# Kernel optimization log

Hardware: AMD Instinct MI355X
Metric: run time of the kernel (lower is better)

Reference implementation:

```python
import jax, jax.numpy as jnp
import numpy as np

D_STATE = 16
D_CONV = 4
EXPAND = 2
GROUPS = 8
EPS = 1e-5


def _layernorm(x, w, b):
    m = x.mean(-1, keepdims=True)
    v = x.var(-1, keepdims=True)
    return (x - m) * jax.lax.rsqrt(v + EPS) * w + b


def _groupnorm(x, w, b):
    B, C = x.shape[:2]
    sp = x.shape[2:]
    xg = x.reshape(B, GROUPS, C // GROUPS, -1)
    m = xg.mean(axis=(2, 3), keepdims=True)
    v = xg.var(axis=(2, 3), keepdims=True)
    xg = (xg - m) * jax.lax.rsqrt(v + EPS)
    x = xg.reshape((B, C) + sp)
    shp = (1, C) + (1,) * len(sp)
    return x * w.reshape(shp) + b.reshape(shp)


def _mamba(xn, in_w, conv_w, conv_b, xp_w, dt_w, dt_b, A_log, Dp, out_w):
    # xn: [B, L, C]
    B, L, C = xn.shape
    di = in_w.shape[0] // 2
    rank = dt_w.shape[1]
    N = D_STATE
    xz = xn @ in_w.T                              # [B, L, 2*di]
    xi, z = xz[..., :di], xz[..., di:]
    # causal depthwise conv1d along L (pad left d_conv-1, truncate to L)
    xc = jnp.moveaxis(xi, 1, 2)                   # [B, di, L]
    xpd = jnp.pad(xc, ((0, 0), (0, 0), (D_CONV - 1, 0)))
    conv = conv_b[None, :, None]
    for k in range(D_CONV):
        conv = conv + conv_w[None, :, k, None] * xpd[:, :, k:k + L]
    u = jnp.moveaxis(jax.nn.silu(conv), 1, 2)     # [B, L, di]
    dbl = u @ xp_w.T                              # [B, L, rank+2N]
    dt = dbl[..., :rank]
    Bm = dbl[..., rank:rank + N]
    Cm = dbl[..., rank + N:]
    delta = jax.nn.softplus(dt @ dt_w.T + dt_b)   # [B, L, di]
    A = -jnp.exp(A_log)                           # [di, N]
    dA = jnp.exp(delta[..., None] * A)            # [B, L, di, N]
    dBu = delta[..., None] * Bm[:, :, None, :] * u[..., None]

    def comb(e1, e2):
        a1, b1 = e1
        a2, b2 = e2
        return a1 * a2, a2 * b1 + b2

    _, h = jax.lax.associative_scan(comb, (dA, dBu), axis=1)  # h_t = dA_t*h_{t-1} + dBu_t
    y = jnp.einsum('bldn,bln->bld', h, Cm) + u * Dp
    y = y * jax.nn.silu(z)
    return y @ out_w.T


def _mamba_layer(x, p):
    B, C = x.shape[:2]
    img = x.shape[2:]
    L = int(np.prod(img))
    xf = jnp.moveaxis(x.reshape(B, C, L), 1, 2)   # [B, L, C]
    xn = _layernorm(xf, p['ln_w'], p['ln_b'])
    xm = _mamba(xn, p['in_w'], p['conv_w'], p['conv_b'], p['xp_w'],
                p['dt_w'], p['dt_b'], p['A_log'], p['Dp'], p['out_w'])
    xm = xm + p['skip'] * xf
    xm = _layernorm(xm, p['ln_w'], p['ln_b'])     # same norm params reused, as in source
    y = xm @ p['proj_w'].T + p['proj_b']
    return jnp.moveaxis(y, 1, 2).reshape((B, C) + img)


def setup_inputs() -> dict:
    key = jax.random.key(0)
    B, C = 2, 48
    img = (16, 32, 32)
    di = EXPAND * C
    rank = -(-C // 16)
    ks = iter(jax.random.split(key, 64))

    def nrm(shape, scale):
        return jax.random.normal(next(ks), shape, jnp.float32) * scale

    inp = {'x': jax.random.normal(next(ks), (B, C) + img, jnp.float32)}
    inp['gn1_w'] = jnp.ones(C); inp['gn1_b'] = jnp.zeros(C)
    inp['gn2_w'] = jnp.ones(C); inp['gn2_b'] = jnp.zeros(C)
    for i in (1, 2):
        inp[f'ln{i}_w'] = jnp.ones(C); inp[f'ln{i}_b'] = jnp.zeros(C)
        inp[f'in_w{i}'] = nrm((2 * di, C), C ** -0.5)
        inp[f'conv_w{i}'] = nrm((di, D_CONV), D_CONV ** -0.5)
        inp[f'conv_b{i}'] = jnp.zeros(di)
        inp[f'xp_w{i}'] = nrm((rank + 2 * D_STATE, di), di ** -0.5)
        inp[f'dt_w{i}'] = nrm((di, rank), rank ** -0.5)
        inp[f'dt_b{i}'] = nrm((di,), 0.1) - 4.0  # softplus -> small positive dt
        inp[f'A_log{i}'] = jnp.log(jnp.tile(jnp.arange(1, D_STATE + 1, dtype=jnp.float32), (di, 1)))
        inp[f'D{i}'] = jnp.ones(di)
        inp[f'out_w{i}'] = nrm((C, di), di ** -0.5)
        inp[f'proj_w{i}'] = nrm((C, C), C ** -0.5)
        inp[f'proj_b{i}'] = jnp.zeros(C)
        inp[f'skip{i}'] = jnp.ones(1)
    return inp


def reference(x, gn1_w, gn1_b, gn2_w, gn2_b,
              ln1_w, ln1_b, in_w1, conv_w1, conv_b1, xp_w1, dt_w1, dt_b1, A_log1, D1, out_w1, proj_w1, proj_b1, skip1,
              ln2_w, ln2_b, in_w2, conv_w2, conv_b2, xp_w2, dt_w2, dt_b2, A_log2, D2, out_w2, proj_w2, proj_b2, skip2):
    p1 = dict(ln_w=ln1_w, ln_b=ln1_b, in_w=in_w1, conv_w=conv_w1, conv_b=conv_b1, xp_w=xp_w1,
              dt_w=dt_w1, dt_b=dt_b1, A_log=A_log1, Dp=D1, out_w=out_w1, proj_w=proj_w1,
              proj_b=proj_b1, skip=skip1)
    p2 = dict(ln_w=ln2_w, ln_b=ln2_b, in_w=in_w2, conv_w=conv_w2, conv_b=conv_b2, xp_w=xp_w2,
              dt_w=dt_w2, dt_b=dt_b2, A_log=A_log2, Dp=D2, out_w=out_w2, proj_w=proj_w2,
              proj_b=proj_b2, skip=skip2)
    identity = x
    h = jax.nn.relu(_groupnorm(x, gn1_w, gn1_b))
    h = _mamba_layer(h, p1)
    h = jax.nn.relu(_groupnorm(h, gn2_w, gn2_b))
    h = _mamba_layer(h, p2)
    return h + identity
```

## Files before the change

kernel.cpp:

```cpp
#include <hip/hip_runtime.h>
#include <hip/hip_bf16.h>

#define LCH   48
#define DI    96
#define LSEQ  16384
#define NB    2
#define NPOS  (NB*LSEQ)
#define NSTATE 16
#define CPG   6
#define EPS   1e-5f
#define NC    128
#define CL    128
#define NCHAIN (NB*DI*NSTATE)
#define TS    32

typedef __hip_bfloat16 bf16;

__device__ __forceinline__ float LDW(const void* p, size_t i, bool f32){
    return f32 ? ((const float*)p)[i] : __bfloat162float(((const bf16*)p)[i]);
}

__device__ __forceinline__ float bf2f(unsigned short h){
    union { unsigned int i; float f; } u; u.i = ((unsigned int)h) << 16; return u.f;
}

__device__ __forceinline__ float4 LDW4(const void* p, size_t i4, bool f32){
    if (f32) return ((const float4*)p)[i4];
    ushort4 v = ((const ushort4*)p)[i4];
    return make_float4(bf2f(v.x), bf2f(v.y), bf2f(v.z), bf2f(v.w));
}

__device__ __forceinline__ float row16_sum(float p){
    union { float f; int i; } u, v;
    u.f = p; v.i = __builtin_amdgcn_mov_dpp(u.i, 0x111, 0xf, 0xf, true); p += v.f;
    u.f = p; v.i = __builtin_amdgcn_mov_dpp(u.i, 0x112, 0xf, 0xf, true); p += v.f;
    u.f = p; v.i = __builtin_amdgcn_mov_dpp(u.i, 0x114, 0xf, 0xf, true); p += v.f;
    u.f = p; v.i = __builtin_amdgcn_mov_dpp(u.i, 0x118, 0xf, 0xf, true); p += v.f;
    return p;
}

__global__ void k_flag(const void* gnw, int* flag, float* __restrict__ acc1, float* __restrict__ acc2){
    int t = threadIdx.x;
    if (t == 0){
        const unsigned short* g = (const unsigned short*)gnw;
        flag[0] = (g[0] == 0x3F80) ? 0 : 1;
    }
    if (t < 32){ acc1[t] = 0.f; acc2[t] = 0.f; }
}

__global__ void k_gnpart_x(const void* __restrict__ x, const int* Fg, float* __restrict__ acc){
    const bool f32 = Fg[0];
    int bg = blockIdx.x >> 4, sl = blockIdx.x & 15;
    int b = bg >> 3, g = bg & 7;
    int tid = threadIdx.x;
    float s = 0.f, q = 0.f;
    for (int c = 0; c < CPG; ++c){
        size_t base = (size_t)(b*LCH + g*CPG + c)*LSEQ + sl*1024;
        float4 v = LDW4(x, base/4 + tid, f32);
        s += v.x; q += v.x*v.x;
        s += v.y; q += v.y*v.y;
        s += v.z; q += v.z*v.z;
        s += v.w; q += v.w*v.w;
    }
    __shared__ float ss[256], sq[256];
    ss[tid] = s; sq[tid] = q; __syncthreads();
    for (int st = 128; st > 0; st >>= 1){
        if (tid < st){ ss[tid] += ss[tid+st]; sq[tid] += sq[tid+st]; }
        __syncthreads();
    }
    if (tid == 0){
        atomicAdd(&acc[bg*2],   ss[0]);
        atomicAdd(&acc[bg*2+1], sq[0]);
    }
}

template<int SRC>
__global__ void k_prepin(const void* __restrict__ src, const int* Fg, const float* __restrict__ acc,
                         const void* gnw, const void* gnb, const void* lnw, const void* lnb,
                         const void* __restrict__ inw,
                         float* __restrict__ xf, float* __restrict__ xi, float* __restrict__ z){
    const bool f32 = Fg[0];
    __shared__ float wl[96*52];
    __shared__ float xl[32*52];
    __shared__ float fl[32*52];
    __shared__ float sst[32];
    int tid = threadIdx.x;
    int part = blockIdx.x & 1;
    int pos0 = (blockIdx.x >> 1)*32;
    int b = pos0 >> 14, l0 = pos0 & (LSEQ-1);
    if (tid < 16){
        float mean = acc[tid*2] / (float)(CPG*LSEQ);
        float var  = acc[tid*2+1] / (float)(CPG*LSEQ) - mean*mean;
        sst[tid*2]   = mean;
        sst[tid*2+1] = rsqrtf(var + EPS);
    }
    for (int i = tid; i < 96*12; i += 256){
        int o = i/12, k4 = i - o*12;
        ((float4*)wl)[o*13+k4] = LDW4(inw, (size_t)part*1152 + i, f32);
    }
    if (SRC == 0){
        for (int i = tid; i < 48*32; i += 256){
            int c = i >> 5, p = i & 31;
            xl[p*52+c] = LDW(src, (size_t)(b*LCH+c)*LSEQ + l0 + p, f32);
        }
    } else {
        const float4* ms4 = (const float4*)src;
        for (int i = tid; i < 32*12; i += 256){
            int p = i/12, c4 = i - p*12;
            ((float4*)xl)[p*13+c4] = ms4[(size_t)pos0*12 + i];
        }
    }
    __syncthreads();
    if (tid < 32){
        float* row  = xl + tid*52;
        float* frow = fl + tid*52;
        float s = 0.f, q = 0.f;
        #pragma unroll
        for (int c = 0; c < LCH; ++c){
            int g = c / CPG;
            float mean = sst[(b*8+g)*2], rs = sst[(b*8+g)*2+1];
            float v = row[c];
            v = (v - mean)*rs*LDW(gnw,c,f32) + LDW(gnb,c,f32);
            v = fmaxf(v, 0.f);
            frow[c] = v; s += v; q += v*v;
        }
        float mean = s / (float)LCH;
        float rs = rsqrtf(q/(float)LCH - mean*mean + EPS);
        #pragma unroll
        for (int c = 0; c < LCH; ++c)
            row[c] = (frow[c]-mean)*rs*LDW(lnw,c,f32) + LDW(lnb,c,f32);
    }
    __syncthreads();
    if (part == 0){
        float4* xf4 = (float4*)xf;
        const float4* fl4 = (const float4*)fl;
        for (int i = tid; i < 32*12; i += 256){
            int p = i/12, c4 = i - p*12;
            xf4[(size_t)pos0*12 + i] = fl4[p*13+c4];
        }
    }
    float* dst = part ? z : xi;
    int o  = tid & 31;
    int pg = tid >> 5;
    const float4* wl4 = (const float4*)wl;
    const float4* xl4 = (const float4*)xl;
    float a0[4] = {0.f,0.f,0.f,0.f};
    float a1[4] = {0.f,0.f,0.f,0.f};
    float a2[4] = {0.f,0.f,0.f,0.f};
    #pragma unroll
    for (int k4 = 0; k4 < 12; ++k4){
        float4 w0 = wl4[ o     *13 + k4];
        float4 w1 = wl4[(o+32)*13 + k4];
        float4 w2 = wl4[(o+64)*13 + k4];
        #pragma unroll
        for (int q = 0; q < 4; ++q){
            float4 xv = xl4[(pg*4+q)*13 + k4];
            a0[q] += xv.x*w0.x; a0[q] += xv.y*w0.y; a0[q] += xv.z*w0.z; a0[q] += xv.w*w0.w;
            a1[q] += xv.x*w1.x; a1[q] += xv.y*w1.y; a1[q] += xv.z*w1.z; a1[q] += xv.w*w1.w;
            a2[q] += xv.x*w2.x; a2[q] += xv.y*w2.y; a2[q] += xv.z*w2.z; a2[q] += xv.w*w2.w;
        }
    }
    #pragma unroll
    for (int q = 0; q < 4; ++q){
        size_t pos = (size_t)(pos0 + pg*4 + q);
        dst[pos*DI + o     ] = a0[q];
        dst[pos*DI + o + 32] = a1[q];
        dst[pos*DI + o + 64] = a2[q];
    }
}

__global__ void k_convdbl(const float* __restrict__ xi, const void* cw, const void* cb,
                          const void* __restrict__ xpw, const void* dtw, const void* dtb,
                          const int* Fg, float* __restrict__ u_g, float* __restrict__ B2,
                          float* __restrict__ C2, float* __restrict__ delta_g){
    const bool f32 = Fg[0];
    __shared__ float xil[35*100];
    __shared__ float wbc[32*100];
    __shared__ float wdt[3*100];
    __shared__ float cwl[96*4];
    __shared__ float cbl[96];
    __shared__ float dtwl[96*3];
    __shared__ float dtbl[96];
    __shared__ float dtl[32*3];
    int tid = threadIdx.x;
    int pos0 = blockIdx.x*32;
    int l0 = pos0 & (LSEQ-1);

    for (int i = tid; i < 32*24; i += 256){
        int o = i/24, k4 = i - o*24;
        int row = (o & 1) ? (19 + (o>>1)) : (3 + (o>>1));
        ((float4*)wbc)[o*25 + k4] = LDW4(xpw, (size_t)row*24 + k4, f32);
    }
    if (tid < 72){
        int o = tid/24, k4 = tid - o*24;
        ((float4*)wdt)[o*25 + k4] = LDW4(xpw, (size_t)o*24 + k4, f32);
    }
    for (int i = tid; i < 96*4; i += 256) cwl[i] = LDW(cw, i, f32);
    if (tid < 96) cbl[tid] = LDW(cb, tid, f32);
    for (int i = tid; i < 96*3; i += 256) dtwl[i] = LDW(dtw, i, f32);
    if (tid >= 128 && tid < 224) dtbl[tid-128] = LDW(dtb, tid-128, f32);
    {
        float4* xv = (float4*)xil;
        const float4* gx = (const float4*)xi;
        for (int i = tid; i < 35*24; i += 256){
            int p = i/24, k4 = i - p*24;
            float4 v = make_float4(0.f, 0.f, 0.f, 0.f);
            if (l0 + p - 3 >= 0) v = gx[(size_t)(pos0-3+p)*24 + k4];
            xv[p*25 + k4] = v;
        }
    }
    __syncthreads();

    float uu[12];
    #pragma unroll
    for (int r = 0; r < 12; ++r){
        int i = tid + 256*r;
        int j = i/96, d = i - j*96;
        float4 cw4 = ((const float4*)cwl)[d];
        float acc = cbl[d];
        acc += cw4.x*xil[(j+0)*100+d];
        acc += cw4.y*xil[(j+1)*100+d];
        acc += cw4.z*xil[(j+2)*100+d];
        acc += cw4.w*xil[(j+3)*100+d];
        uu[r] = acc / (1.f + __expf(-acc));
    }
    __syncthreads();

    #pragma unroll
    for (int r = 0; r < 12; ++r){
        int i = tid + 256*r;
        int j = i/96, d = i - j*96;
        xil[j*100+d] = uu[r];
        u_g[(size_t)pos0*DI + i] = uu[r];
    }
    __syncthreads();

    {
        int o  = tid & 31;
        int pg = ((tid>>6)<<1) | ((tid>>5)&1);
        const float4* ulv = (const float4*)xil;
        const float4* wv  = (const float4*)wbc;
        float a0=0.f, a1=0.f, a2=0.f, a3=0.f;
        #pragma unroll 4
        for (int k4 = 0; k4 < 24; ++k4){
            float4 u0 = ulv[(pg*4+0)*25 + k4];
            float4 u1 = ulv[(pg*4+1)*25 + k4];
            float4 u2 = ulv[(pg*4+2)*25 + k4];
            float4 u3 = ulv[(pg*4+3)*25 + k4];
            float4 w  = wv[o*25 + k4];
            a0 += u0.x*w.x; a0 += u0.y*w.y; a0 += u0.z*w.z; a0 += u0.w*w.w;
            a1 += u1.x*w.x; a1 += u1.y*w.y; a1 += u1.z*w.z; a1 += u1.w*w.w;
            a2 += u2.x*w.x; a2 += u2.y*w.y; a2 += u2.z*w.z; a2 += u2.w*w.w;
            a3 += u3.x*w.x; a3 += u3.y*w.y; a3 += u3.z*w.z; a3 += u3.w*w.w;
        }
        int nn = o >> 1;
        float* dst = (o & 1) ? C2 : B2;
        size_t pb = (size_t)(pos0 + pg*4);
        dst[(pb+0)*16 + nn] = a0;
        dst[(pb+1)*16 + nn] = a1;
        dst[(pb+2)*16 + nn] = a2;
        dst[(pb+3)*16 + nn] = a3;
    }
    if (tid < 96){
        int o = tid >> 5;
        int p = tid & 31;
        const float4* ulv = (const float4*)xil;
        const float4* wv  = (const float4*)wdt;
        float a = 0.f;
        #pragma unroll 4
        for (int k4 = 0; k4 < 24; ++k4){
            float4 uv = ulv[p*25 + k4];
            float4 w  = wv[o*25 + k4];
            a += uv.x*w.x; a += uv.y*w.y; a += uv.z*w.z; a += uv.w*w.w;
        }
        dtl[p*3+o] = a;
    }
    __syncthreads();

    for (int i = tid; i < 32*96; i += 256){
        int p = i/96, d = i - p*96;
        float acc = dtbl[d];
        #pragma unroll
        for (int r = 0; r < 3; ++r) acc += dtl[p*3+r]*dtwl[d*3+r];
        float sp = (acc > 20.f) ? acc : log1pf(__expf(acc));
        delta_g[(size_t)pos0*DI + i] = sp;
    }
}

__global__ void k_scanA(const float* __restrict__ delta, const float* __restrict__ u,
                        const float* __restrict__ B2, const void* Alog, const int* Fg,
                        float* __restrict__ Pb, float* __restrict__ Sb){
    const bool f32 = Fg[0];
    __shared__ float dls[2][TS*16];
    __shared__ float uus[2][TS*16];
    __shared__ float bbs[2][TS*16];
    int tid = threadIdx.x;
    int t = blockIdx.x*256 + tid;
    int n = tid & 15;
    int sg0 = blockIdx.x*16;
    int cb2 = sg0/96;
    int d0 = sg0 - cb2*96;
    int b = cb2 & 1, chunk = cb2 >> 1;
    int dloc = tid >> 4;
    int d = d0 + dloc;
    float An = -__expf(LDW(Alog, d*16+n, f32));
    float P = 1.f, S = 0.f;
    int base = b*LSEQ + chunk*CL;
    int si0 = tid >> 4, sj = tid & 15;
    int si1 = si0 + 16;
    float pd0, pd1, pu0, pu1, pb0, pb1;
    auto fetch = [&](int tb){
        pd0 = delta[(size_t)(tb+si0)*DI + d0 + sj];
        pu0 = u    [(size_t)(tb+si0)*DI + d0 + sj];
        pb0 = B2   [(size_t)(tb+si0)*16 + sj];
        pd1 = delta[(size_t)(tb+si1)*DI + d0 + sj];
        pu1 = u    [(size_t)(tb+si1)*DI + d0 + sj];
        pb1 = B2   [(size_t)(tb+si1)*16 + sj];
    };
    auto store = [&](int bs){
        dls[bs][tid] = pd0; dls[bs][tid+256] = pd1;
        uus[bs][tid] = pu0; uus[bs][tid+256] = pu1;
        bbs[bs][tid] = pb0; bbs[bs][tid+256] = pb1;
    };
    fetch(base); store(0);
    __syncthreads();
    for (int tile = 0; tile < CL/TS; ++tile){
        int cur = tile & 1;
        if (tile+1 < CL/TS) fetch(base + (tile+1)*TS);
        #pragma unroll
        for (int i = 0; i < TS; ++i){
            float dl = dls[cur][i*16 + dloc];
            float uu = uus[cur][i*16 + dloc];
            float Bn = bbs[cur][i*16 + n];
            float a = __expf(dl*An);
            P *= a;
            S = a*S + dl*Bn*uu;
        }
        if (tile+1 < CL/TS) store(1-cur);
        __syncthreads();
    }
    Pb[t] = P; Sb[t] = S;
}

__global__ void k_scanB(const float* __restrict__ Pb, const float* __restrict__ Sb,
                        float* __restrict__ carry){
    int ch = blockIdx.x*blockDim.x + threadIdx.x;
    float c = 0.f;
    for (int cb = 0; cb < NC; cb += 8){
        float P[8], S[8];
        #pragma unroll
        for (int j = 0; j < 8; ++j){
            P[j] = Pb[(size_t)(cb+j)*NCHAIN + ch];
            S[j] = Sb[(size_t)(cb+j)*NCHAIN + ch];
        }
        #pragma unroll
        for (int j = 0; j < 8; ++j){
            carry[(size_t)(cb+j)*NCHAIN + ch] = c;
            c = S[j] + P[j]*c;
        }
    }
}

__global__ void k_scanC(const float* __restrict__ delta, const float* __restrict__ u,
                        const float* __restrict__ B2, const float* __restrict__ C2,
                        const float* __restrict__ carry, const void* Alog, const void* Dp,
                        const int* Fg, float* __restrict__ y){
    const bool f32 = Fg[0];
    __shared__ float dls[2][TS*16];
    __shared__ float uus[2][TS*16];
    __shared__ float bbs[2][TS*16];
    __shared__ float ccs[2][TS*16];
    int tid = threadIdx.x;
    int n = tid & 15;
    int sg0 = blockIdx.x*16;
    int cb2 = sg0/96;
    int d0 = sg0 - cb2*96;
    int b = cb2 & 1, chunk = cb2 >> 1;
    int dloc = tid >> 4;
    int d = d0 + dloc;
    float An = -__expf(LDW(Alog, d*16+n, f32));
    float Dpd = LDW(Dp, d, f32);
    float h = carry[chunk*NCHAIN + (b*DI+d)*NSTATE + n];
    int base = b*LSEQ + chunk*CL;
    int si0 = tid >> 4, sj = tid & 15;
    int si1 = si0 + 16;
    float pd0, pd1, pu0, pu1, pb0, pb1, pc0, pc1;
    auto fetch = [&](int tb){
        pd0 = delta[(size_t)(tb+si0)*DI + d0 + sj];
        pu0 = u    [(size_t)(tb+si0)*DI + d0 + sj];
        pb0 = B2   [(size_t)(tb+si0)*16 + sj];
        pc0 = C2   [(size_t)(tb+si0)*16 + sj];
        pd1 = delta[(size_t)(tb+si1)*DI + d0 + sj];
        pu1 = u    [(size_t)(tb+si1)*DI + d0 + sj];
        pb1 = B2   [(size_t)(tb+si1)*16 + sj];
        pc1 = C2   [(size_t)(tb+si1)*16 + sj];
    };
    auto store = [&](int bs){
        dls[bs][tid] = pd0; dls[bs][tid+256] = pd1;
        uus[bs][tid] = pu0; uus[bs][tid+256] = pu1;
        bbs[bs][tid] = pb0; bbs[bs][tid+256] = pb1;
        ccs[bs][tid] = pc0; ccs[bs][tid+256] = pc1;
    };
    fetch(base); store(0);
    __syncthreads();
    for (int tile = 0; tile < CL/TS; ++tile){
        int cur = tile & 1;
        int tb = base + tile*TS;
        if (tile+1 < CL/TS) fetch(base + (tile+1)*TS);
        #pragma unroll
        for (int i = 0; i < TS; ++i){
            float dl = dls[cur][i*16 + dloc];
            float uu = uus[cur][i*16 + dloc];
            float Bn = bbs[cur][i*16 + n];
            float Cn = ccs[cur][i*16 + n];
            float a = __expf(dl*An);
            h = a*h + dl*Bn*uu;
            float p = row16_sum(h*Cn);
            if (n == 15) y[(size_t)(tb+i)*DI + d] = p + uu*Dpd;
        }
        if (tile+1 < CL/TS) store(1-cur);
        __syncthreads();
    }
}

__global__ void k_outproj(const float* __restrict__ psum, const void* __restrict__ outw,
                          const void* skipv, const int* Fg,
                          const float* __restrict__ zx,
                          const float* __restrict__ xf, float* __restrict__ xm){
    const bool f32 = Fg[0];
    __shared__ float wl[48*100];
    __shared__ float yl[32*100];
    int tid = threadIdx.x;
    int pos0 = blockIdx.x*32;
    for (int i = tid; i < 48*24; i += 256){
        int o = i/24, k4 = i - o*24;
        ((float4*)wl)[o*25+k4] = LDW4(outw, i, f32);
    }
    {
        const float4* ps4 = (const float4*)psum;
        const float4* zz4 = (const float4*)zx;
        for (int i = tid; i < 32*24; i += 256){
            int p = i/24, k4 = i - p*24;
            float4 pv = ps4[(size_t)pos0*24 + i];
            float4 zv = zz4[(size_t)pos0*24 + i];
            float4 y;
            y.x = pv.x * (zv.x / (1.f + __expf(-zv.x)));
            y.y = pv.y * (zv.y / (1.f + __expf(-zv.y)));
            y.z = pv.z * (zv.z / (1.f + __expf(-zv.z)));
            y.w = pv.w * (zv.w / (1.f + __expf(-zv.w)));
            ((float4*)yl)[p*25+k4] = y;
        }
    }
    __syncthreads();
    float sk = LDW(skipv, 0, f32);
    int os = tid & 63;
    int pofs = tid >> 6;
    const float4* wl4 = (const float4*)wl;
    const float4* yl4 = (const float4*)yl;
    float a[2][4] = {{0.f,0.f,0.f,0.f},{0.f,0.f,0.f,0.f}};
    if (os < 48){
        #pragma unroll 4
        for (int k4 = 0; k4 < 24; ++k4){
            float4 w = wl4[os*25+k4];
            #pragma unroll
            for (int j = 0; j < 2; ++j){
                int p0 = pofs + j*16;
                #pragma unroll
                for (int q = 0; q < 4; ++q){
                    float4 y = yl4[(p0+q*4)*25+k4];
                    a[j][q] += y.x*w.x; a[j][q] += y.y*w.y; a[j][q] += y.z*w.z; a[j][q] += y.w*w.w;
                }
            }
        }
        #pragma unroll
        for (int j = 0; j < 2; ++j){
            int p0 = pofs + j*16;
            #pragma unroll
            for (int q = 0; q < 4; ++q){
                size_t oi = (size_t)(pos0+p0+q*4)*LCH + os;
                xm[oi] = a[j][q] + sk*xf[oi];
            }
        }
    }
}

template<int FIN>
__global__ void k_lnproj(const float* __restrict__ xm, const void* lnw, const void* lnb,
                         const void* __restrict__ pw, const void* pb, const int* Fg,
                         const void* __restrict__ xres, float* __restrict__ mout,
                         float* __restrict__ acc2, void* __restrict__ outp){
    const bool f32 = Fg[0];
    __shared__ float wp[48*52];
    __shared__ float xl[32*52];
    __shared__ float ol[32*49];
    __shared__ float gs[48], gq[48];
    int tid = threadIdx.x;
    int pos0 = blockIdx.x*32;
    if (FIN == 0 && tid < 48){ gs[tid] = 0.f; gq[tid] = 0.f; }
    for (int i = tid; i < 48*12; i += 256){
        int o = i/12, k4 = i - o*12;
        ((float4*)wp)[o*13+k4] = LDW4(pw, i, f32);
    }
    {
        const float4* xm4 = (const float4*)xm;
        for (int i = tid; i < 32*12; i += 256){
            int p = i/12, c4 = i - p*12;
            ((float4*)xl)[p*13+c4] = xm4[(size_t)pos0*12 + i];
        }
    }
    __syncthreads();
    if (tid < 32){
        float* row = xl + tid*52;
        float s = 0.f, q = 0.f;
        #pragma unroll
        for (int c = 0; c < LCH; ++c){ float v = row[c]; s += v; q += v*v; }
        float mean = s / (float)LCH;
        float rs = rsqrtf(q/(float)LCH - mean*mean + EPS);
        #pragma unroll
        for (int c = 0; c < LCH; ++c)
            row[c] = (row[c]-mean)*rs*LDW(lnw,c,f32) + LDW(lnb,c,f32);
    }
    __syncthreads();
    int os = tid & 63;
    int pofs = tid >> 6;
    float bias = (os < 48) ? LDW(pb, os, f32) : 0.f;
    const float4* wp4 = (const float4*)wp;
    const float4* xl4 = (const float4*)xl;
    float sl = 0.f, ql = 0.f;
    float a[2][4] = {{bias,bias,bias,bias},{bias,bias,bias,bias}};
    if (os < 48){
        #pragma unroll 4
        for (int k4 = 0; k4 < 12; ++k4){
            float4 w = wp4[os*13+k4];
            #pragma unroll
            for (int j = 0; j < 2; ++j){
                int p0 = pofs + j*16;
                #pragma unroll
                for (int q = 0; q < 4; ++q){
                    float4 x = xl4[(p0+q*4)*13+k4];
                    a[j][q] += x.x*w.x; a[j][q] += x.y*w.y; a[j][q] += x.z*w.z; a[j][q] += x.w*w.w;
                }
            }
        }
        #pragma unroll
        for (int j = 0; j < 2; ++j){
            int p0 = pofs + j*16;
            #pragma unroll
            for (int q = 0; q < 4; ++q){
                if (FIN == 0){
                    mout[(size_t)(pos0+p0+q*4)*LCH + os] = a[j][q];
                    sl += a[j][q]; ql += a[j][q]*a[j][q];
                } else {
                    ol[(p0+q*4)*49 + os] = a[j][q];
                }
            }
        }
    }
    if (FIN == 0){
        if (os < 48){ atomicAdd(&gs[os], sl); atomicAdd(&gq[os], ql); }
        __syncthreads();
        if (tid < 8){
            int b = pos0 >> 14;
            float s = 0.f, q = 0.f;
            #pragma unroll
            for (int c = 0; c < CPG; ++c){ s += gs[tid*CPG+c]; q += gq[tid*CPG+c]; }
            atomicAdd(&acc2[(b*8+tid)*2],   s);
            atomicAdd(&acc2[(b*8+tid)*2+1], q);
        }
    } else {
        __syncthreads();
        int b = pos0 >> 14, l0 = pos0 & (LSEQ-1);
        for (int i = tid; i < 48*32; i += 256){
            int c = i >> 5, p = i & 31;
            size_t gi = (size_t)(b*LCH+c)*LSEQ + l0 + p;
            float v = ol[p*49+c] + LDW(xres, gi, f32);
            if (f32) ((float*)outp)[gi] = v;
            else     ((bf16*)outp)[gi] = __float2bfloat16(v);
        }
    }
}

extern "C" void kernel_launch(void* const* d_in, const int* in_sizes, int n_in,
                              void* d_out, int out_size, void* d_ws, size_t ws_size,
                              hipStream_t stream){
    const void* x = d_in[0];
    auto W = [&](int i){ return (const void*)d_in[i]; };

    float* ws = (float*)d_ws;
    size_t off = 0;
    int*   flag  = (int*)ws;  off += 16;
    float* acc1  = ws + off;  off += 32;
    float* acc2  = ws + off;  off += 32;
    float* xf    = ws + off;  off += (size_t)NPOS*LCH;
    float* xi    = ws + off;  off += (size_t)NPOS*DI;
    float* zb    = ws + off;  off += (size_t)NPOS*DI;
    float* ub    = ws + off;  off += (size_t)NPOS*DI;
    float* B2    = ws + off;  off += (size_t)NPOS*16;
    float* C2    = ws + off;  off += (size_t)NPOS*16;
    float* Pb    = ws + off;  off += (size_t)NC*NCHAIN;
    float* Sb    = ws + off;  off += (size_t)NC*NCHAIN;
    float* carry = ws + off;  off += (size_t)NC*NCHAIN;
    float* delta = ws + off;  off += (size_t)NPOS*DI;
    float* mbuf  = ws + off;  off += (size_t)NPOS*LCH;
    float* ybuf  = xi;
    float* xmbuf = delta;

    k_flag<<<1, 64, 0, stream>>>(W(1), flag, acc1, acc2);

    k_gnpart_x<<<256, 256, 0, stream>>>(x, flag, acc1);
    k_prepin<0><<<2*NPOS/32, 256, 0, stream>>>(x, flag, acc1, W(1), W(2), W(5), W(6), W(7), xf, xi, zb);
    k_convdbl<<<NPOS/32, 256, 0, stream>>>(xi, W(8), W(9), W(10), W(11), W(12), flag, ub, B2, C2, delta);
    k_scanA<<<NC*NCHAIN/256, 256, 0, stream>>>(delta, ub, B2, W(13), flag, Pb, Sb);
    k_scanB<<<NCHAIN/256, 256, 0, stream>>>(Pb, Sb, carry);
    k_scanC<<<NC*NCHAIN/256, 256, 0, stream>>>(delta, ub, B2, C2, carry, W(13), W(14), flag, ybuf);
    k_outproj<<<NPOS/32, 256, 0, stream>>>(ybuf, W(15), W(18), flag, zb, xf, xmbuf);
    k_lnproj<0><<<NPOS/32, 256, 0, stream>>>(xmbuf, W(5), W(6), W(16), W(17), flag, nullptr, mbuf, acc2, nullptr);

    k_prepin<1><<<2*NPOS/32, 256, 0, stream>>>(mbuf, flag, acc2, W(3), W(4), W(19), W(20), W(21), xf, xi, zb);
    k_convdbl<<<NPOS/32, 256, 0, stream>>>(xi, W(22), W(23), W(24), W(25), W(26), flag, ub, B2, C2, delta);
    k_scanA<<<NC*NCHAIN/256, 256, 0, stream>>>(delta, ub, B2, W(27), flag, Pb, Sb);
    k_scanB<<<NCHAIN/256, 256, 0, stream>>>(Pb, Sb, carry);
    k_scanC<<<NC*NCHAIN/256, 256, 0, stream>>>(delta, ub, B2, C2, carry, W(27), W(28), flag, ybuf);
    k_outproj<<<NPOS/32, 256, 0, stream>>>(ybuf, W(29), W(32), flag, zb, xf, xmbuf);
    k_lnproj<1><<<NPOS/32, 256, 0, stream>>>(xmbuf, W(19), W(20), W(30), W(31), flag, x, nullptr, nullptr, d_out);
}
```

Measured before the change: 446.2 us.

## Transpose scan shared tiles for float4 reads and remap projection thread tiling

The chunked scan kernels now store their staging tiles transposed (channel-major with padded stride 36), so each thread reads four timesteps per float4 LDS load instead of four scalar loads. Separately, the out-projection and proj kernels switch from a 64-wide thread layout that left a quarter of the threads idle to a 16x16 mapping where each thread computes three outputs for two positions. This keeps every thread busy and raises weight reuse per LDS load. The transposed store pattern may add LDS bank conflicts on writes, and the new GEMM tiling changes register use and global store coalescing.

```diff
diff --git a/kernel.cpp b/kernel.cpp
--- a/kernel.cpp
+++ b/kernel.cpp
@@ -13,6 +13,7 @@
 #define CL    128
 #define NCHAIN (NB*DI*NSTATE)
 #define TS    32
+#define TSS   36
 
 typedef __hip_bfloat16 bf16;
 
@@ -291,9 +292,9 @@
                         const float* __restrict__ B2, const void* Alog, const int* Fg,
                         float* __restrict__ Pb, float* __restrict__ Sb){
     const bool f32 = Fg[0];
-    __shared__ float dls[2][TS*16];
-    __shared__ float uus[2][TS*16];
-    __shared__ float bbs[2][TS*16];
+    __shared__ float dls[2][16*TSS];
+    __shared__ float uus[2][16*TSS];
+    __shared__ float bbs[2][16*TSS];
     int tid = threadIdx.x;
     int t = blockIdx.x*256 + tid;
     int n = tid & 15;
@@ -318,9 +319,9 @@
         pb1 = B2   [(size_t)(tb+si1)*16 + sj];
     };
     auto store = [&](int bs){
-        dls[bs][tid] = pd0; dls[bs][tid+256] = pd1;
-        uus[bs][tid] = pu0; uus[bs][tid+256] = pu1;
-        bbs[bs][tid] = pb0; bbs[bs][tid+256] = pb1;
+        dls[bs][sj*TSS+si0] = pd0; dls[bs][sj*TSS+si1] = pd1;
+        uus[bs][sj*TSS+si0] = pu0; uus[bs][sj*TSS+si1] = pu1;
+        bbs[bs][sj*TSS+si0] = pb0; bbs[bs][sj*TSS+si1] = pb1;
     };
     fetch(base); store(0);
     __syncthreads();
@@ -328,13 +329,15 @@
         int cur = tile & 1;
         if (tile+1 < CL/TS) fetch(base + (tile+1)*TS);
         #pragma unroll
-        for (int i = 0; i < TS; ++i){
-            float dl = dls[cur][i*16 + dloc];
-            float uu = uus[cur][i*16 + dloc];
-            float Bn = bbs[cur][i*16 + n];
-            float a = __expf(dl*An);
-            P *= a;
-            S = a*S + dl*Bn*uu;
+        for (int i4 = 0; i4 < TS/4; ++i4){
+            float4 dl4 = *(const float4*)&dls[cur][dloc*TSS + i4*4];
+            float4 uu4 = *(const float4*)&uus[cur][dloc*TSS + i4*4];
+            float4 bn4 = *(const float4*)&bbs[cur][n   *TSS + i4*4];
+            float a;
+            a = __expf(dl4.x*An); P *= a; S = a*S + dl4.x*bn4.x*uu4.x;
+            a = __expf(dl4.y*An); P *= a; S = a*S + dl4.y*bn4.y*uu4.y;
+            a = __expf(dl4.z*An); P *= a; S = a*S + dl4.z*bn4.z*uu4.z;
+            a = __expf(dl4.w*An); P *= a; S = a*S + dl4.w*bn4.w*uu4.w;
         }
         if (tile+1 < CL/TS) store(1-cur);
         __syncthreads();
@@ -366,10 +369,10 @@
                         const float* __restrict__ carry, const void* Alog, const void* Dp,
                         const int* Fg, float* __restrict__ y){
     const bool f32 = Fg[0];
-    __shared__ float dls[2][TS*16];
-    __shared__ float uus[2][TS*16];
-    __shared__ float bbs[2][TS*16];
-    __shared__ float ccs[2][TS*16];
+    __shared__ float dls[2][16*TSS];
+    __shared__ float uus[2][16*TSS];
+    __shared__ float bbs[2][16*TSS];
+    __shared__ float ccs[2][16*TSS];
     int tid = threadIdx.x;
     int n = tid & 15;
     int sg0 = blockIdx.x*16;
@@ -396,10 +399,10 @@
         pc1 = C2   [(size_t)(tb+si1)*16 + sj];
     };
     auto store = [&](int bs){
-        dls[bs][tid] = pd0; dls[bs][tid+256] = pd1;
-        uus[bs][tid] = pu0; uus[bs][tid+256] = pu1;
-        bbs[bs][tid] = pb0; bbs[bs][tid+256] = pb1;
-        ccs[bs][tid] = pc0; ccs[bs][tid+256] = pc1;
+        dls[bs][sj*TSS+si0] = pd0; dls[bs][sj*TSS+si1] = pd1;
+        uus[bs][sj*TSS+si0] = pu0; uus[bs][sj*TSS+si1] = pu1;
+        bbs[bs][sj*TSS+si0] = pb0; bbs[bs][sj*TSS+si1] = pb1;
+        ccs[bs][sj*TSS+si0] = pc0; ccs[bs][sj*TSS+si1] = pc1;
     };
     fetch(base); store(0);
     __syncthreads();
@@ -408,15 +411,24 @@
         int tb = base + tile*TS;
         if (tile+1 < CL/TS) fetch(base + (tile+1)*TS);
         #pragma unroll
-        for (int i = 0; i < TS; ++i){
-            float dl = dls[cur][i*16 + dloc];
-            float uu = uus[cur][i*16 + dloc];
-            float Bn = bbs[cur][i*16 + n];
-            float Cn = ccs[cur][i*16 + n];
-            float a = __expf(dl*An);
-            h = a*h + dl*Bn*uu;
-            float p = row16_sum(h*Cn);
-            if (n == 15) y[(size_t)(tb+i)*DI + d] = p + uu*Dpd;
+        for (int i4 = 0; i4 < TS/4; ++i4){
+            float4 dl4 = *(const float4*)&dls[cur][dloc*TSS + i4*4];
+            float4 uu4 = *(const float4*)&uus[cur][dloc*TSS + i4*4];
+            float4 bn4 = *(const float4*)&bbs[cur][n   *TSS + i4*4];
+            float4 cn4 = *(const float4*)&ccs[cur][n   *TSS + i4*4];
+            float a, p;
+            a = __expf(dl4.x*An); h = a*h + dl4.x*bn4.x*uu4.x;
+            p = row16_sum(h*cn4.x);
+            if (n == 15) y[(size_t)(tb+i4*4+0)*DI + d] = p + uu4.x*Dpd;
+            a = __expf(dl4.y*An); h = a*h + dl4.y*bn4.y*uu4.y;
+            p = row16_sum(h*cn4.y);
+            if (n == 15) y[(size_t)(tb+i4*4+1)*DI + d] = p + uu4.y*Dpd;
+            a = __expf(dl4.z*An); h = a*h + dl4.z*bn4.z*uu4.z;
+            p = row16_sum(h*cn4.z);
+            if (n == 15) y[(size_t)(tb+i4*4+2)*DI + d] = p + uu4.z*Dpd;
+            a = __expf(dl4.w*An); h = a*h + dl4.w*bn4.w*uu4.w;
+            p = row16_sum(h*cn4.w);
+            if (n == 15) y[(size_t)(tb+i4*4+3)*DI + d] = p + uu4.w*Dpd;
         }
         if (tile+1 < CL/TS) store(1-cur);
         __syncthreads();
@@ -453,33 +465,31 @@
     }
     __syncthreads();
     float sk = LDW(skipv, 0, f32);
-    int os = tid & 63;
-    int pofs = tid >> 6;
+    int o16 = tid & 15;
+    int pg  = tid >> 4;
     const float4* wl4 = (const float4*)wl;
     const float4* yl4 = (const float4*)yl;
-    float a[2][4] = {{0.f,0.f,0.f,0.f},{0.f,0.f,0.f,0.f}};
-    if (os < 48){
-        #pragma unroll 4
-        for (int k4 = 0; k4 < 24; ++k4){
-            float4 w = wl4[os*25+k4];
-            #pragma unroll
-            for (int j = 0; j < 2; ++j){
-                int p0 = pofs + j*16;
-                #pragma unroll
-                for (int q = 0; q < 4; ++q){
-                    float4 y = yl4[(p0+q*4)*25+k4];
-                    a[j][q] += y.x*w.x; a[j][q] += y.y*w.y; a[j][q] += y.z*w.z; a[j][q] += y.w*w.w;
-                }
-            }
-        }
-        #pragma unroll
-        for (int j = 0; j < 2; ++j){
-            int p0 = pofs + j*16;
-            #pragma unroll
-            for (int q = 0; q < 4; ++q){
-                size_t oi = (size_t)(pos0+p0+q*4)*LCH + os;
-                xm[oi] = a[j][q] + sk*xf[oi];
-            }
+    float a[3][2] = {{0.f,0.f},{0.f,0.f},{0.f,0.f}};
+    #pragma unroll 4
+    for (int k4 = 0; k4 < 24; ++k4){
+        float4 w0 = wl4[ o16     *25+k4];
+        float4 w1 = wl4[(o16+16)*25+k4];
+        float4 w2 = wl4[(o16+32)*25+k4];
+        float4 y0 = yl4[(pg*2+0)*25+k4];
+        float4 y1 = yl4[(pg*2+1)*25+k4];
+        a[0][0] += y0.x*w0.x; a[0][0] += y0.y*w0.y; a[0][0] += y0.z*w0.z; a[0][0] += y0.w*w0.w;
+        a[0][1] += y1.x*w0.x; a[0][1] += y1.y*w0.y; a[0][1] += y1.z*w0.z; a[0][1] += y1.w*w0.w;
+        a[1][0] += y0.x*w1.x; a[1][0] += y0.y*w1.y; a[1][0] += y0.z*w1.z; a[1][0] += y0.w*w1.w;
+        a[1][1] += y1.x*w1.x; a[1][1] += y1.y*w1.y; a[1][1] += y1.z*w1.z; a[1][1] += y1.w*w1.w;
+        a[2][0] += y0.x*w2.x; a[2][0] += y0.y*w2.y; a[2][0] += y0.z*w2.z; a[2][0] += y0.w*w2.w;
+        a[2][1] += y1.x*w2.x; a[2][1] += y1.y*w2.y; a[2][1] += y1.z*w2.z; a[2][1] += y1.w*w2.w;
+    }
+    #pragma unroll
+    for (int r = 0; r < 3; ++r){
+        #pragma unroll
+        for (int q = 0; q < 2; ++q){
+            size_t oi = (size_t)(pos0+pg*2+q)*LCH + o16 + r*16;
+            xm[oi] = a[r][q] + sk*xf[oi];
         }
     }
 }
@@ -521,43 +531,44 @@
             row[c] = (row[c]-mean)*rs*LDW(lnw,c,f32) + LDW(lnb,c,f32);
     }
     __syncthreads();
-    int os = tid & 63;
-    int pofs = tid >> 6;
-    float bias = (os < 48) ? LDW(pb, os, f32) : 0.f;
+    int o16 = tid & 15;
+    int pg  = tid >> 4;
+    float b0 = LDW(pb, o16,      f32);
+    float b1 = LDW(pb, o16 + 16, f32);
+    float b2 = LDW(pb, o16 + 32, f32);
     const float4* wp4 = (const float4*)wp;
     const float4* xl4 = (const float4*)xl;
-    float sl = 0.f, ql = 0.f;
-    float a[2][4] = {{bias,bias,bias,bias},{bias,bias,bias,bias}};
-    if (os < 48){
-        #pragma unroll 4
-        for (int k4 = 0; k4 < 12; ++k4){
-            float4 w = wp4[os*13+k4];
+    float a[3][2] = {{b0,b0},{b1,b1},{b2,b2}};
+    #pragma unroll 4
+    for (int k4 = 0; k4 < 12; ++k4){
+        float4 w0 = wp4[ o16     *13+k4];
+        float4 w1 = wp4[(o16+16)*13+k4];
+        float4 w2 = wp4[(o16+32)*13+k4];
+        float4 x0 = xl4[(pg*2+0)*13+k4];
+        float4 x1 = xl4[(pg*2+1)*13+k4];
+        a[0][0] += x0.x*w0.x; a[0][0] += x0.y*w0.y; a[0][0] += x0.z*w0.z; a[0][0] += x0.w*w0.w;
+        a[0][1] += x1.x*w0.x; a[0][1] += x1.y*w0.y; a[0][1] += x1.z*w0.z; a[0][1] += x1.w*w0.w;
+        a[1][0] += x0.x*w1.x; a[1][0] += x0.y*w1.y; a[1][0] += x0.z*w1.z; a[1][0] += x0.w*w1.w;
+        a[1][1] += x1.x*w1.x; a[1][1] += x1.y*w1.y; a[1][1] += x1.z*w1.z; a[1][1] += x1.w*w1.w;
+        a[2][0] += x0.x*w2.x; a[2][0] += x0.y*w2.y; a[2][0] += x0.z*w2.z; a[2][0] += x0.w*w2.w;
+        a[2][1] += x1.x*w2.x; a[2][1] += x1.y*w2.y; a[2][1] += x1.z*w2.z; a[2][1] += x1.w*w2.w;
+    }
+    if (FIN == 0){
+        float sl[3] = {0.f,0.f,0.f}, ql[3] = {0.f,0.f,0.f};
+        #pragma unroll
+        for (int r = 0; r < 3; ++r){
             #pragma unroll
-            for (int j = 0; j < 2; ++j){
-                int p0 = pofs + j*16;
-                #pragma unroll
-                for (int q = 0; q < 4; ++q){
-                    float4 x = xl4[(p0+q*4)*13+k4];
-                    a[j][q] += x.x*w.x; a[j][q] += x.y*w.y; a[j][q] += x.z*w.z; a[j][q] += x.w*w.w;
-                }
+            for (int q = 0; q < 2; ++q){
+                float v = a[r][q];
+                mout[(size_t)(pos0+pg*2+q)*LCH + o16 + r*16] = v;
+                sl[r] += v; ql[r] += v*v;
             }
         }
         #pragma unroll
-        for (int j = 0; j < 2; ++j){
-            int p0 = pofs + j*16;
-            #pragma unroll
-            for (int q = 0; q < 4; ++q){
-                if (FIN == 0){
-                    mout[(size_t)(pos0+p0+q*4)*LCH + os] = a[j][q];
-                    sl += a[j][q]; ql += a[j][q]*a[j][q];
-                } else {
-                    ol[(p0+q*4)*49 + os] = a[j][q];
-                }
-            }
-        }
-    }
-    if (FIN == 0){
-        if (os < 48){ atomicAdd(&gs[os], sl); atomicAdd(&gq[os], ql); }
+        for (int r = 0; r < 3; ++r){
+            atomicAdd(&gs[o16 + r*16], sl[r]);
+            atomicAdd(&gq[o16 + r*16], ql[r]);
+        }
         __syncthreads();
         if (tid < 8){
             int b = pos0 >> 14;
@@ -568,6 +579,12 @@
             atomicAdd(&acc2[(b*8+tid)*2+1], q);
         }
     } else {
+        #pragma unroll
+        for (int r = 0; r < 3; ++r){
+            #pragma unroll
+            for (int q = 0; q < 2; ++q)
+                ol[(pg*2+q)*49 + o16 + r*16] = a[r][q];
+        }
         __syncthreads();
         int b = pos0 >> 14, l0 = pos0 & (LSEQ-1);
         for (int i = tid; i < 48*32; i += 256){
```

New measurement: 433.1 us. -2.9%, faster.
